# Kernel tuning notes

Hardware: AMD Instinct MI355X
Metric: run time of the kernel (lower is better)

Reference implementation:

```python
import jax, jax.numpy as jnp
import numpy as np

N_NODES = 100000
N_EDGES = 1600000
S_FEAT = 16   # static node features
D_FEAT = 8    # dynamic node features
E_FEAT = 4    # edge features
K = 2
EDGE_IN = E_FEAT + 2 * S_FEAT + 2 * D_FEAT  # 52
HIDDEN = 2 * D_FEAT                          # 16


def setup_inputs() -> dict:
    key = jax.random.key(0)
    ks = jax.random.split(key, 12)
    inp = {
        "x_s": jax.random.normal(ks[0], (N_NODES, S_FEAT), jnp.float32),
        "x_d": jax.random.normal(ks[1], (N_NODES, D_FEAT), jnp.float32),
        "edge_attr": jax.random.normal(ks[2], (N_EDGES, E_FEAT), jnp.float32),
        # edge MLP: Linear(EDGE_IN->HIDDEN) + ReLU + Linear(HIDDEN->D_FEAT)
        "W1": jax.random.normal(ks[3], (HIDDEN, EDGE_IN), jnp.float32) / np.sqrt(EDGE_IN),
        "b1": jnp.zeros((HIDDEN,), jnp.float32),
        "W2": jax.random.normal(ks[4], (D_FEAT, HIDDEN), jnp.float32) / np.sqrt(HIDDEN),
        "b2": jnp.zeros((D_FEAT,), jnp.float32),
        # K+1 = 3 filter matrices, Linear(D->D, bias=False): y = x @ W.T
        "Wf0": jax.random.normal(ks[5], (D_FEAT, D_FEAT), jnp.float32) / np.sqrt(D_FEAT),
        "Wf1": jax.random.normal(ks[6], (D_FEAT, D_FEAT), jnp.float32) / np.sqrt(D_FEAT),
        "Wf2": jax.random.normal(ks[7], (D_FEAT, D_FEAT), jnp.float32) / np.sqrt(D_FEAT),
        "edge_index": jax.random.randint(ks[8], (2, N_EDGES), 0, N_NODES, jnp.int64
                                         if jax.config.jax_enable_x64 else jnp.int32),
    }
    return inp


def _edge_mlp(e, W1, b1, W2, b2):
    h = jax.nn.relu(e @ W1.T + b1)
    return h @ W2.T + b2


def reference(x_s, x_d, edge_attr, W1, b1, W2, b2, Wf0, Wf1, Wf2, edge_index):
    row, col = edge_index[0], edge_index[1]
    num_nodes = x_d.shape[0]

    # s_ij depends only on static inputs (x_s, x_d, edge_attr), not on `out`,
    # so it is identical across the K steps; compute it once. The per-step
    # boolean edge mask is applied multiplicatively below, which matches the
    # torch masked-gather/scatter exactly (normalization is per-edge).
    e_ij = jnp.concatenate(
        [x_s[row], x_s[col], x_d[row], x_d[col], edge_attr], axis=1)  # [E, 52]
    s_ij = _edge_mlp(e_ij, W1, b1, W2, b2)                            # [E, D]
    nrm = jnp.linalg.norm(s_ij, axis=1, keepdims=True)
    s_ij = jnp.where(nrm > 0, s_ij / jnp.where(nrm > 0, nrm, 1.0), 0.0)

    filters = [Wf0, Wf1, Wf2]
    out = x_d @ filters[0].T
    for k in range(K):
        mask = out.sum(1) != 0                         # [N]
        edge_mask = (mask[row] | mask[col]).astype(out.dtype)  # [E]
        hydraulic_gradient = out[col] - out[row]       # [E, D]
        shift_sum = hydraulic_gradient * s_ij * edge_mask[:, None]
        scattered = jax.ops.segment_sum(shift_sum, col, num_segments=num_nodes)
        scattered = scattered @ filters[k + 1].T
        out = out + scattered
    return out
```

## Files before the change

kernel.cpp:

```cpp
#include <hip/hip_runtime.h>
#include <hip/hip_fp16.h>

#define S_FEAT 16
#define D_FEAT 8
#define E_FEAT 4
#define EDGE_IN 52
#define HIDDEN 16
#define SCAN_CHUNK 2048

__device__ __forceinline__ void mlp_sij(
    const float* __restrict__ x_s, const float* __restrict__ x_d,
    const float* __restrict__ edge_attr,
    const float* __restrict__ W1, const float* __restrict__ b1,
    const float* __restrict__ W2, const float* __restrict__ b2,
    int row, int col, int e, float s[D_FEAT])
{
    float in[EDGE_IN];
    {
        const float4* p = (const float4*)(x_s + (size_t)row * S_FEAT);
#pragma unroll
        for (int q = 0; q < 4; ++q) {
            float4 v = p[q];
            in[q * 4 + 0] = v.x; in[q * 4 + 1] = v.y;
            in[q * 4 + 2] = v.z; in[q * 4 + 3] = v.w;
        }
    }
    {
        const float4* p = (const float4*)(x_s + (size_t)col * S_FEAT);
#pragma unroll
        for (int q = 0; q < 4; ++q) {
            float4 v = p[q];
            in[16 + q * 4 + 0] = v.x; in[16 + q * 4 + 1] = v.y;
            in[16 + q * 4 + 2] = v.z; in[16 + q * 4 + 3] = v.w;
        }
    }
    {
        const float4* p = (const float4*)(x_d + (size_t)row * D_FEAT);
#pragma unroll
        for (int q = 0; q < 2; ++q) {
            float4 v = p[q];
            in[32 + q * 4 + 0] = v.x; in[32 + q * 4 + 1] = v.y;
            in[32 + q * 4 + 2] = v.z; in[32 + q * 4 + 3] = v.w;
        }
    }
    {
        const float4* p = (const float4*)(x_d + (size_t)col * D_FEAT);
#pragma unroll
        for (int q = 0; q < 2; ++q) {
            float4 v = p[q];
            in[40 + q * 4 + 0] = v.x; in[40 + q * 4 + 1] = v.y;
            in[40 + q * 4 + 2] = v.z; in[40 + q * 4 + 3] = v.w;
        }
    }
    {
        float4 v = *(const float4*)(edge_attr + (size_t)e * E_FEAT);
        in[48] = v.x; in[49] = v.y; in[50] = v.z; in[51] = v.w;
    }

    float h[HIDDEN];
#pragma unroll
    for (int i = 0; i < HIDDEN; ++i) {
        float acc = b1[i];
#pragma unroll
        for (int j = 0; j < EDGE_IN; ++j)
            acc = fmaf(in[j], W1[i * EDGE_IN + j], acc);
        h[i] = acc > 0.f ? acc : 0.f;
    }

    float nrm2 = 0.f;
#pragma unroll
    for (int i = 0; i < D_FEAT; ++i) {
        float acc = b2[i];
#pragma unroll
        for (int j = 0; j < HIDDEN; ++j)
            acc = fmaf(h[j], W2[i * HIDDEN + j], acc);
        s[i] = acc;
        nrm2 = fmaf(acc, acc, nrm2);
    }
    float nrm = sqrtf(nrm2);
    float inv = nrm > 0.f ? 1.f / nrm : 0.f;
#pragma unroll
    for (int i = 0; i < D_FEAT; ++i) s[i] *= inv;
}

__global__ __launch_bounds__(256) void zero_counts_kernel(int* __restrict__ counts, int N)
{
    int i = blockIdx.x * blockDim.x + threadIdx.x;
    if (i < N) counts[i] = 0;
}

__global__ __launch_bounds__(256) void hist_kernel(
    const int* __restrict__ ei, int E, int N, int* __restrict__ counts)
{
    int e = blockIdx.x * blockDim.x + threadIdx.x;
    if (e >= E) return;
    int col = ei[E + e];
    atomicAdd(&counts[col], 1);
}

__global__ __launch_bounds__(256) void scan_local_kernel(
    const int* __restrict__ counts, int* __restrict__ partial,
    int* __restrict__ blocksums, int N)
{
    __shared__ int sh[256];
    int b = blockIdx.x, t = threadIdx.x;
    int base = b * SCAN_CHUNK + t * 8;
    int v[8];
    int run = 0;
#pragma unroll
    for (int j = 0; j < 8; ++j) {
        int c = (base + j < N) ? counts[base + j] : 0;
        v[j] = run;
        run += c;
    }
    sh[t] = run;
    __syncthreads();
#pragma unroll
    for (int st = 1; st < 256; st <<= 1) {
        int x = (t >= st) ? sh[t - st] : 0;
        __syncthreads();
        sh[t] += x;
        __syncthreads();
    }
    int excl = sh[t] - run;
    if (t == 255) blocksums[b] = sh[255];
#pragma unroll
    for (int j = 0; j < 8; ++j)
        if (base + j < N) partial[base + j] = excl + v[j];
}

__global__ void scan_blk_kernel(int* __restrict__ blocksums, int NB)
{
    if (threadIdx.x == 0) {
        int run = 0;
        for (int i = 0; i < NB; ++i) { int c = blocksums[i]; blocksums[i] = run; run += c; }
    }
}

__global__ __launch_bounds__(256) void scan_add_kernel(
    int* __restrict__ offsets, int* __restrict__ cursor,
    const int* __restrict__ blocksums, int N, int E)
{
    int i = blockIdx.x * blockDim.x + threadIdx.x;
    if (i < N) {
        int off = offsets[i] + blocksums[i / SCAN_CHUNK];
        offsets[i] = off;
        cursor[i]  = off;
    } else if (i == N) {
        offsets[N] = E;
    }
}

__global__ __launch_bounds__(256) void mlp_scatter_kernel(
    const float* __restrict__ x_s, const float* __restrict__ x_d,
    const float* __restrict__ edge_attr,
    const float* __restrict__ W1, const float* __restrict__ b1,
    const float* __restrict__ W2, const float* __restrict__ b2,
    const int* __restrict__ ei, int E,
    int* __restrict__ cursor, __half* __restrict__ s_srt, int* __restrict__ row_srt)
{
    int e = blockIdx.x * blockDim.x + threadIdx.x;
    if (e >= E) return;
    int row = ei[e], col = ei[E + e];
    float s[D_FEAT];
    mlp_sij(x_s, x_d, edge_attr, W1, b1, W2, b2, row, col, e, s);
    int pos = atomicAdd(&cursor[col], 1);
    __half h[8];
#pragma unroll
    for (int i = 0; i < 8; ++i) h[i] = __float2half(s[i]);
    *(float4*)(s_srt + (size_t)pos * 8) = *(const float4*)h;
    row_srt[pos] = row;
}

__global__ __launch_bounds__(256) void node_init_kernel(
    const float* __restrict__ x_d, const float* __restrict__ Wf0,
    float* __restrict__ out, unsigned char* __restrict__ mask, int N)
{
    int n = blockIdx.x * blockDim.x + threadIdx.x;
    if (n >= N) return;
    float xd[D_FEAT];
    {
        const float4* p = (const float4*)(x_d + (size_t)n * D_FEAT);
        float4 a = p[0], b = p[1];
        xd[0] = a.x; xd[1] = a.y; xd[2] = a.z; xd[3] = a.w;
        xd[4] = b.x; xd[5] = b.y; xd[6] = b.z; xd[7] = b.w;
    }
    float o[D_FEAT];
    float rs = 0.f;
#pragma unroll
    for (int i = 0; i < D_FEAT; ++i) {
        float acc = 0.f;
#pragma unroll
        for (int j = 0; j < D_FEAT; ++j)
            acc = fmaf(xd[j], Wf0[i * D_FEAT + j], acc);
        o[i] = acc;
        rs += acc;
    }
    float4* op = (float4*)(out + (size_t)n * D_FEAT);
    op[0] = make_float4(o[0], o[1], o[2], o[3]);
    op[1] = make_float4(o[4], o[5], o[6], o[7]);
    mask[n] = (rs != 0.f) ? 1 : 0;
}

__global__ __launch_bounds__(256) void csr_step_kernel(
    const float* __restrict__ out_in, float* __restrict__ out_out,
    const unsigned char* __restrict__ mask_in, unsigned char* __restrict__ mask_out,
    const int* __restrict__ offsets, const int* __restrict__ row_srt,
    const __half* __restrict__ s_srt, const float* __restrict__ Wf, int N)
{
    int lane = threadIdx.x & 63;
    int node = blockIdx.x * 4 + (threadIdx.x >> 6);
    if (node >= N) return;
    int e_sub = lane >> 3, f = lane & 7;
    int beg = offsets[node], end = offsets[node + 1];
    float outc = out_in[(size_t)node * 8 + f];
    int mc = mask_in[node];
    float acc = 0.f;
    for (int base = beg; base < end; base += 8) {
        int e = base + e_sub;
        bool valid = e < end;
        int row = valid ? row_srt[e] : node;
        float s = valid ? __half2float(s_srt[(size_t)e * 8 + f]) : 0.f;
        float outr = out_in[(size_t)row * 8 + f];
        int m = mc | (int)mask_in[row];
        acc += (m != 0) ? (outc - outr) * s : 0.f;
    }
    acc += __shfl_xor(acc, 8);
    acc += __shfl_xor(acc, 16);
    acc += __shfl_xor(acc, 32);
    float upd = 0.f;
#pragma unroll
    for (int j = 0; j < 8; ++j) {
        float aj = __shfl(acc, (lane & ~7) | j);
        upd = fmaf(Wf[f * 8 + j], aj, upd);
    }
    float o = outc + upd;
    float rs = o;
    rs += __shfl_xor(rs, 1);
    rs += __shfl_xor(rs, 2);
    rs += __shfl_xor(rs, 4);
    if (e_sub == 0) {
        out_out[(size_t)node * 8 + f] = o;
        if (f == 0) mask_out[node] = (rs != 0.f) ? 1 : 0;
    }
}

__global__ __launch_bounds__(256) void fb_node_init_kernel(
    const float* __restrict__ x_d, const float* __restrict__ Wf0,
    float* __restrict__ out, float* __restrict__ scattered, int N)
{
    int n = blockIdx.x * blockDim.x + threadIdx.x;
    if (n >= N) return;
    float xd[D_FEAT];
    const float4* p = (const float4*)(x_d + (size_t)n * D_FEAT);
    float4 a = p[0], b = p[1];
    xd[0] = a.x; xd[1] = a.y; xd[2] = a.z; xd[3] = a.w;
    xd[4] = b.x; xd[5] = b.y; xd[6] = b.z; xd[7] = b.w;
    float o[D_FEAT];
#pragma unroll
    for (int i = 0; i < D_FEAT; ++i) {
        float acc = 0.f;
#pragma unroll
        for (int j = 0; j < D_FEAT; ++j)
            acc = fmaf(xd[j], Wf0[i * D_FEAT + j], acc);
        o[i] = acc;
    }
    float4* op = (float4*)(out + (size_t)n * D_FEAT);
    op[0] = make_float4(o[0], o[1], o[2], o[3]);
    op[1] = make_float4(o[4], o[5], o[6], o[7]);
    float4* sp = (float4*)(scattered + (size_t)n * D_FEAT);
    sp[0] = make_float4(0.f, 0.f, 0.f, 0.f);
    sp[1] = make_float4(0.f, 0.f, 0.f, 0.f);
}

__global__ __launch_bounds__(256) void fb_edge_step_kernel(
    const float* __restrict__ x_s, const float* __restrict__ x_d,
    const float* __restrict__ edge_attr,
    const float* __restrict__ W1, const float* __restrict__ b1,
    const float* __restrict__ W2, const float* __restrict__ b2,
    const float* __restrict__ out,
    const int* __restrict__ ei, int E, float* __restrict__ scattered)
{
    int e = blockIdx.x * blockDim.x + threadIdx.x;
    if (e >= E) return;
    int row = ei[e], col = ei[E + e];
    const float4* pr = (const float4*)(out + (size_t)row * D_FEAT);
    const float4* pc = (const float4*)(out + (size_t)col * D_FEAT);
    float4 r0 = pr[0], r1 = pr[1], c0 = pc[0], c1 = pc[1];
    float srow = r0.x + r0.y + r0.z + r0.w + r1.x + r1.y + r1.z + r1.w;
    float scol = c0.x + c0.y + c0.z + c0.w + c1.x + c1.y + c1.z + c1.w;
    if (srow == 0.f && scol == 0.f) return;
    float s[D_FEAT];
    mlp_sij(x_s, x_d, edge_attr, W1, b1, W2, b2, row, col, e, s);
    float* dst = scattered + (size_t)col * D_FEAT;
    atomicAdd(dst + 0, (c0.x - r0.x) * s[0]);
    atomicAdd(dst + 1, (c0.y - r0.y) * s[1]);
    atomicAdd(dst + 2, (c0.z - r0.z) * s[2]);
    atomicAdd(dst + 3, (c0.w - r0.w) * s[3]);
    atomicAdd(dst + 4, (c1.x - r1.x) * s[4]);
    atomicAdd(dst + 5, (c1.y - r1.y) * s[5]);
    atomicAdd(dst + 6, (c1.z - r1.z) * s[6]);
    atomicAdd(dst + 7, (c1.w - r1.w) * s[7]);
}

__global__ __launch_bounds__(256) void fb_node_update_kernel(
    float* __restrict__ out, float* __restrict__ scattered,
    const float* __restrict__ Wf, int N)
{
    int n = blockIdx.x * blockDim.x + threadIdx.x;
    if (n >= N) return;
    float sc[D_FEAT];
    float4* sp = (float4*)(scattered + (size_t)n * D_FEAT);
    float4 a = sp[0], b = sp[1];
    sc[0] = a.x; sc[1] = a.y; sc[2] = a.z; sc[3] = a.w;
    sc[4] = b.x; sc[5] = b.y; sc[6] = b.z; sc[7] = b.w;
    sp[0] = make_float4(0.f, 0.f, 0.f, 0.f);
    sp[1] = make_float4(0.f, 0.f, 0.f, 0.f);
    float4* op = (float4*)(out + (size_t)n * D_FEAT);
    float4 o0 = op[0], o1 = op[1];
    float o[D_FEAT] = {o0.x, o0.y, o0.z, o0.w, o1.x, o1.y, o1.z, o1.w};
#pragma unroll
    for (int i = 0; i < D_FEAT; ++i) {
        float acc = 0.f;
#pragma unroll
        for (int j = 0; j < D_FEAT; ++j)
            acc = fmaf(sc[j], Wf[i * D_FEAT + j], acc);
        o[i] += acc;
    }
    op[0] = make_float4(o[0], o[1], o[2], o[3]);
    op[1] = make_float4(o[4], o[5], o[6], o[7]);
}

extern "C" void kernel_launch(void* const* d_in, const int* in_sizes, int n_in,
                              void* d_out, int out_size, void* d_ws, size_t ws_size,
                              hipStream_t stream) {
    const float* x_s       = (const float*)d_in[0];
    const float* x_d       = (const float*)d_in[1];
    const float* edge_attr = (const float*)d_in[2];
    const float* W1        = (const float*)d_in[3];
    const float* b1        = (const float*)d_in[4];
    const float* W2        = (const float*)d_in[5];
    const float* b2        = (const float*)d_in[6];
    const float* Wf[3]     = {(const float*)d_in[7], (const float*)d_in[8],
                              (const float*)d_in[9]};
    const int*   ei        = (const int*)d_in[10];

    const int N = in_sizes[1] / D_FEAT;
    const int E = in_sizes[10] / 2;

    float* out = (float*)d_out;

    size_t off = 0;
    auto carve = [&](size_t bytes) { size_t p = off; off = (off + bytes + 255) & ~255ULL; return p; };
    size_t o_counts  = carve((size_t)(N + 1) * 4);
    size_t o_offsets = carve((size_t)(N + 1) * 4);
    size_t o_cursor  = carve((size_t)(N + 1) * 4);
    size_t o_bsums   = carve(256 * 4);
    size_t o_maskA   = carve((size_t)N);
    size_t o_maskB   = carve((size_t)N);
    size_t o_bufA    = carve((size_t)N * D_FEAT * 4);
    size_t o_rowsrt  = carve((size_t)E * 4);
    size_t o_ssrt    = carve((size_t)E * D_FEAT * 2);
    const size_t need = off;

    dim3 blk(256);
    dim3 gE((E + 255) / 256);
    dim3 gN((N + 255) / 256);

    if (ws_size >= need) {
        char* ws = (char*)d_ws;
        int*   counts  = (int*)(ws + o_counts);
        int*   offsets = (int*)(ws + o_offsets);
        int*   cursor  = (int*)(ws + o_cursor);
        int*   bsums   = (int*)(ws + o_bsums);
        unsigned char* maskA = (unsigned char*)(ws + o_maskA);
        unsigned char* maskB = (unsigned char*)(ws + o_maskB);
        float* bufA    = (float*)(ws + o_bufA);
        int*   row_srt = (int*)(ws + o_rowsrt);
        __half* s_srt  = (__half*)(ws + o_ssrt);

        const int NB = (N + SCAN_CHUNK - 1) / SCAN_CHUNK;

        zero_counts_kernel<<<gN, blk, 0, stream>>>(counts, N);
        hist_kernel<<<gE, blk, 0, stream>>>(ei, E, N, counts);
        scan_local_kernel<<<dim3(NB), blk, 0, stream>>>(counts, offsets, bsums, N);
        scan_blk_kernel<<<dim3(1), dim3(64), 0, stream>>>(bsums, NB);
        scan_add_kernel<<<dim3((N + 256) / 256), blk, 0, stream>>>(offsets, cursor, bsums, N, E);

        node_init_kernel<<<gN, blk, 0, stream>>>(x_d, Wf[0], out, maskA, N);
        mlp_scatter_kernel<<<gE, blk, 0, stream>>>(
            x_s, x_d, edge_attr, W1, b1, W2, b2, ei, E, cursor, s_srt, row_srt);

        dim3 gC((N + 3) / 4);
        csr_step_kernel<<<gC, blk, 0, stream>>>(
            out, bufA, maskA, maskB, offsets, row_srt, s_srt, Wf[1], N);
        csr_step_kernel<<<gC, blk, 0, stream>>>(
            bufA, out, maskB, maskA, offsets, row_srt, s_srt, Wf[2], N);
    } else {
        float* scattered = (float*)d_ws;
        fb_node_init_kernel<<<gN, blk, 0, stream>>>(x_d, Wf[0], out, scattered, N);
        for (int k = 0; k < 2; ++k) {
            fb_edge_step_kernel<<<gE, blk, 0, stream>>>(
                x_s, x_d, edge_attr, W1, b1, W2, b2, out, ei, E, scattered);
            fb_node_update_kernel<<<gN, blk, 0, stream>>>(out, scattered, Wf[k + 1], N);
        }
    }
}
```

Before: 435.4 us.

## Pack edge weights as 12-bit fixed point with row into 16-byte records

```diff
diff --git a/kernel.cpp b/kernel.cpp
--- a/kernel.cpp
+++ b/kernel.cpp
@@ -1,5 +1,4 @@
 #include <hip/hip_runtime.h>
-#include <hip/hip_fp16.h>
 
 #define S_FEAT 16
 #define D_FEAT 8
@@ -7,6 +6,9 @@
 #define EDGE_IN 52
 #define HIDDEN 16
 #define SCAN_CHUNK 2048
+#define NSUB 8
+
+typedef unsigned int uint4v __attribute__((ext_vector_type(4)));
 
 __device__ __forceinline__ void mlp_sij(
     const float* __restrict__ x_s, const float* __restrict__ x_d,
@@ -83,23 +85,50 @@
     for (int i = 0; i < D_FEAT; ++i) s[i] *= inv;
 }
 
-__global__ __launch_bounds__(256) void zero_counts_kernel(int* __restrict__ counts, int N)
+__device__ __forceinline__ uint4v pack_rec(const float s[8], int row)
+{
+    int q[8];
+#pragma unroll
+    for (int i = 0; i < 8; ++i) {
+        float v = fminf(fmaxf(s[i] * 2047.f, -2047.f), 2047.f);
+        q[i] = (int)rintf(v) & 0xFFF;
+    }
+    uint4v r;
+    r[0] = (unsigned)(q[0] | (q[1] << 12) | (q[2] << 24));
+    r[1] = (unsigned)((q[2] >> 8) | (q[3] << 4) | (q[4] << 16) | (q[5] << 28));
+    r[2] = (unsigned)((q[5] >> 4) | (q[6] << 8) | (q[7] << 20));
+    r[3] = (unsigned)row;
+    return r;
+}
+
+__device__ __forceinline__ float rec_s(uint4v r, int f)
+{
+    int off = f * 12;
+    unsigned lo = off < 32 ? r[0] : (off < 64 ? r[1] : r[2]);
+    unsigned hi = off < 32 ? r[1] : (off < 64 ? r[2] : 0u);
+    unsigned sh = (unsigned)off & 31u;
+    unsigned long long both = ((unsigned long long)hi << 32) | lo;
+    int q = ((int)((unsigned)(both >> sh) << 20)) >> 20;
+    return (float)q * (1.f / 2047.f);
+}
+
+__global__ __launch_bounds__(256) void zero_counts_kernel(int* __restrict__ counts, int M)
 {
     int i = blockIdx.x * blockDim.x + threadIdx.x;
-    if (i < N) counts[i] = 0;
+    if (i < M) counts[i] = 0;
 }
 
 __global__ __launch_bounds__(256) void hist_kernel(
-    const int* __restrict__ ei, int E, int N, int* __restrict__ counts)
+    const int* __restrict__ ei, int E, int N, int* __restrict__ counts8)
 {
     int e = blockIdx.x * blockDim.x + threadIdx.x;
     if (e >= E) return;
     int col = ei[E + e];
-    atomicAdd(&counts[col], 1);
+    atomicAdd(&counts8[(threadIdx.x & (NSUB - 1)) * N + col], 1);
 }
 
 __global__ __launch_bounds__(256) void scan_local_kernel(
-    const int* __restrict__ counts, int* __restrict__ partial,
+    const int* __restrict__ counts8, int* __restrict__ partial,
     int* __restrict__ blocksums, int N)
 {
     __shared__ int sh[256];
@@ -109,7 +138,12 @@
     int run = 0;
 #pragma unroll
     for (int j = 0; j < 8; ++j) {
-        int c = (base + j < N) ? counts[base + j] : 0;
+        int c = 0;
+        if (base + j < N) {
+#pragma unroll
+            for (int s8 = 0; s8 < NSUB; ++s8)
+                c += counts8[s8 * N + base + j];
+        }
         v[j] = run;
         run += c;
     }
@@ -157,19 +191,16 @@
     const float* __restrict__ W1, const float* __restrict__ b1,
     const float* __restrict__ W2, const float* __restrict__ b2,
     const int* __restrict__ ei, int E,
-    int* __restrict__ cursor, __half* __restrict__ s_srt, int* __restrict__ row_srt)
+    int* __restrict__ cursor, uint4v* __restrict__ recs)
 {
     int e = blockIdx.x * blockDim.x + threadIdx.x;
     if (e >= E) return;
     int row = ei[e], col = ei[E + e];
     float s[D_FEAT];
     mlp_sij(x_s, x_d, edge_attr, W1, b1, W2, b2, row, col, e, s);
+    uint4v rec = pack_rec(s, row);
     int pos = atomicAdd(&cursor[col], 1);
-    __half h[8];
-#pragma unroll
-    for (int i = 0; i < 8; ++i) h[i] = __float2half(s[i]);
-    *(float4*)(s_srt + (size_t)pos * 8) = *(const float4*)h;
-    row_srt[pos] = row;
+    __builtin_nontemporal_store(rec, recs + pos);
 }
 
 __global__ __launch_bounds__(256) void node_init_kernel(
@@ -205,8 +236,8 @@
 __global__ __launch_bounds__(256) void csr_step_kernel(
     const float* __restrict__ out_in, float* __restrict__ out_out,
     const unsigned char* __restrict__ mask_in, unsigned char* __restrict__ mask_out,
-    const int* __restrict__ offsets, const int* __restrict__ row_srt,
-    const __half* __restrict__ s_srt, const float* __restrict__ Wf, int N)
+    const int* __restrict__ offsets, const uint4v* __restrict__ recs,
+    const float* __restrict__ Wf, int N)
 {
     int lane = threadIdx.x & 63;
     int node = blockIdx.x * 4 + (threadIdx.x >> 6);
@@ -219,8 +250,10 @@
     for (int base = beg; base < end; base += 8) {
         int e = base + e_sub;
         bool valid = e < end;
-        int row = valid ? row_srt[e] : node;
-        float s = valid ? __half2float(s_srt[(size_t)e * 8 + f]) : 0.f;
+        uint4v rec = (uint4v)(0u);
+        if (valid) rec = __builtin_nontemporal_load(recs + e);
+        int row = (int)rec[3];
+        float s = rec_s(rec, f);
         float outr = out_in[(size_t)row * 8 + f];
         int m = mc | (int)mask_in[row];
         acc += (m != 0) ? (outc - outr) * s : 0.f;
@@ -352,15 +385,14 @@
 
     size_t off = 0;
     auto carve = [&](size_t bytes) { size_t p = off; off = (off + bytes + 255) & ~255ULL; return p; };
-    size_t o_counts  = carve((size_t)(N + 1) * 4);
+    size_t o_counts  = carve((size_t)NSUB * N * 4);
     size_t o_offsets = carve((size_t)(N + 1) * 4);
     size_t o_cursor  = carve((size_t)(N + 1) * 4);
     size_t o_bsums   = carve(256 * 4);
     size_t o_maskA   = carve((size_t)N);
     size_t o_maskB   = carve((size_t)N);
     size_t o_bufA    = carve((size_t)N * D_FEAT * 4);
-    size_t o_rowsrt  = carve((size_t)E * 4);
-    size_t o_ssrt    = carve((size_t)E * D_FEAT * 2);
+    size_t o_recs    = carve((size_t)E * 16);
     const size_t need = off;
 
     dim3 blk(256);
@@ -369,33 +401,32 @@
 
     if (ws_size >= need) {
         char* ws = (char*)d_ws;
-        int*   counts  = (int*)(ws + o_counts);
+        int*   counts8 = (int*)(ws + o_counts);
         int*   offsets = (int*)(ws + o_offsets);
         int*   cursor  = (int*)(ws + o_cursor);
         int*   bsums   = (int*)(ws + o_bsums);
         unsigned char* maskA = (unsigned char*)(ws + o_maskA);
         unsigned char* maskB = (unsigned char*)(ws + o_maskB);
         float* bufA    = (float*)(ws + o_bufA);
-        int*   row_srt = (int*)(ws + o_rowsrt);
-        __half* s_srt  = (__half*)(ws + o_ssrt);
+        uint4v* recs   = (uint4v*)(ws + o_recs);
 
         const int NB = (N + SCAN_CHUNK - 1) / SCAN_CHUNK;
 
-        zero_counts_kernel<<<gN, blk, 0, stream>>>(counts, N);
-        hist_kernel<<<gE, blk, 0, stream>>>(ei, E, N, counts);
-        scan_local_kernel<<<dim3(NB), blk, 0, stream>>>(counts, offsets, bsums, N);
+        zero_counts_kernel<<<dim3((NSUB * N + 255) / 256), blk, 0, stream>>>(counts8, NSUB * N);
+        hist_kernel<<<gE, blk, 0, stream>>>(ei, E, N, counts8);
+        scan_local_kernel<<<dim3(NB), blk, 0, stream>>>(counts8, offsets, bsums, N);
         scan_blk_kernel<<<dim3(1), dim3(64), 0, stream>>>(bsums, NB);
         scan_add_kernel<<<dim3((N + 256) / 256), blk, 0, stream>>>(offsets, cursor, bsums, N, E);
 
         node_init_kernel<<<gN, blk, 0, stream>>>(x_d, Wf[0], out, maskA, N);
         mlp_scatter_kernel<<<gE, blk, 0, stream>>>(
-            x_s, x_d, edge_attr, W1, b1, W2, b2, ei, E, cursor, s_srt, row_srt);
+            x_s, x_d, edge_attr, W1, b1, W2, b2, ei, E, cursor, recs);
 
         dim3 gC((N + 3) / 4);
         csr_step_kernel<<<gC, blk, 0, stream>>>(
-            out, bufA, maskA, maskB, offsets, row_srt, s_srt, Wf[1], N);
+            out, bufA, maskA, maskB, offsets, recs, Wf[1], N);
         csr_step_kernel<<<gC, blk, 0, stream>>>(
-            bufA, out, maskB, maskA, offsets, row_srt, s_srt, Wf[2], N);
+            bufA, out, maskB, maskA, offsets, recs, Wf[2], N);
     } else {
         float* scattered = (float*)d_ws;
         fb_node_init_kernel<<<gN, blk, 0, stream>>>(x_d, Wf[0], out, scattered, N);
```

Result: faster. 419.7 us (-3.6%).
